# Optimization experiments

Hardware: AMD Instinct MI355X
Metric: run time of the kernel (lower is better)

## Reference

```python
import jax, jax.numpy as jnp
import numpy as np

B, T, E = 2, 2048, 1024
H, D = 16, 64
FF = 4096
EPS = 1e-5


def _layer_norm(x, g, b):
    m = jnp.mean(x, axis=-1, keepdims=True)
    v = jnp.mean(jnp.square(x - m), axis=-1, keepdims=True)
    return (x - m) * jax.lax.rsqrt(v + EPS) * g + b


def setup_inputs() -> dict:
    key = jax.random.key(0)
    ks = jax.random.split(key, 8)
    s = lambda fan_in: 1.0 / np.sqrt(fan_in)
    return {
        "src": jax.random.normal(ks[0], (B, T, E), jnp.float32),
        "Wq": jax.random.normal(ks[1], (E, E), jnp.float32) * s(E),
        "Wk": jax.random.normal(ks[2], (E, E), jnp.float32) * s(E),
        "Wv": jax.random.normal(ks[3], (E, E), jnp.float32) * s(E),
        "Wo": jax.random.normal(ks[4], (E, E), jnp.float32) * s(E),
        "W1": jax.random.normal(ks[5], (2 * FF, E), jnp.float32) * s(E),
        "b1": jnp.zeros((2 * FF,), jnp.float32),
        "W2": jax.random.normal(ks[6], (E, FF), jnp.float32) * s(FF),
        "b2": jnp.zeros((E,), jnp.float32),
        "ln1_w": jnp.ones((E,), jnp.float32),
        "ln1_b": jnp.zeros((E,), jnp.float32),
        "ln2_w": jnp.ones((E,), jnp.float32),
        "ln2_b": jnp.zeros((E,), jnp.float32),
    }


def reference(src, Wq, Wk, Wv, Wo, W1, b1, W2, b2, ln1_w, ln1_b, ln2_w, ln2_b):
    # --- pre-norm self-attention block ---
    h = _layer_norm(src, ln1_w, ln1_b)                       # [B,T,E]
    q = (h @ Wq.T).reshape(B, T, H, D)                       # [B,T,H,D]
    k = (h @ Wk.T).reshape(B, T, H, D)
    v = (h @ Wv.T).reshape(B, T, H, D)
    scores = jnp.einsum("bqhd,bkhd->bhqk", q, k) / np.sqrt(D)
    probs = jax.nn.softmax(scores, axis=-1)                  # [B,H,T,T]
    attn = jnp.einsum("bhqk,bkhd->bqhd", probs, v).reshape(B, T, E)
    x = src + attn @ Wo.T                                    # residual (dropout=0)
    # --- pre-norm GEGLU FFN block ---
    h2 = _layer_norm(x, ln2_w, ln2_b)
    u = h2 @ W1.T + b1                                       # [B,T,2*FF]
    a, gates = jnp.split(u, 2, axis=-1)
    f = a * jax.nn.gelu(gates, approximate=False)            # GEGLU (exact erf gelu)
    return x + (f @ W2.T + b2)
```

## Files before the change

kernel.cpp:

```cpp
#include <hip/hip_runtime.h>
#include <stdint.h>
#include <math.h>

#define DEVI __device__ __forceinline__

typedef __attribute__((ext_vector_type(8))) short sv8;
typedef __attribute__((ext_vector_type(4))) short sv4;
typedef __attribute__((ext_vector_type(4))) float fv4;

typedef __attribute__((address_space(1))) void av1_t;
typedef __attribute__((address_space(3))) void av3_t;

constexpr int Bb = 2, Tt = 2048, Ee = 1024, Hh = 16, Dd = 64, FFd = 4096;
constexpr int NN = Bb * Tt;
constexpr float EPSv = 1e-5f;

#define WAIT_VM(n) asm volatile("s_waitcnt vmcnt(" #n ")" ::: "memory")

DEVI float b2f(unsigned short s) {
  union { unsigned u; float f; } v; v.u = ((unsigned)s) << 16; return v.f;
}
DEVI unsigned short f2b(float f) {
  union { float f; unsigned u; } v; v.f = f;
  return (unsigned short)((v.u + 0x7FFFu + ((v.u >> 16) & 1u)) >> 16);
}
DEVI unsigned short f2b_rtz(float f) {
  union { float f; unsigned u; } v; v.f = f;
  return (unsigned short)(v.u >> 16);
}

DEVI void load_lds16(const void* g, void* s) {
  __builtin_amdgcn_global_load_lds((av1_t*)(unsigned long long)g,
                                   (av3_t*)(unsigned)(unsigned long long)s,
                                   16, 0, 0);
}

__global__ __launch_bounds__(256) void cvt_kernel(const float* __restrict__ in,
                                                  unsigned short* __restrict__ out, int n,
                                                  float scale) {
  int i = (blockIdx.x * 256 + threadIdx.x) * 4;
  if (i >= n) return;
  float4 v = *(const float4*)(in + i);
  sv4 o;
  o[0] = (short)f2b(v.x * scale); o[1] = (short)f2b(v.y * scale);
  o[2] = (short)f2b(v.z * scale); o[3] = (short)f2b(v.w * scale);
  *(sv4*)(out + i) = o;
}

__global__ __launch_bounds__(256) void cvt_w1_kernel(const float* __restrict__ in,
                                                     unsigned short* __restrict__ out) {
  int i = (blockIdx.x * 256 + threadIdx.x) * 4;
  const int r = i >> 10, c = i & 1023;
  const int rp = (r < FFd) ? ((r >> 4) * 32 + (r & 15))
                           : (((r - FFd) >> 4) * 32 + 16 + (r & 15));
  float4 v = *(const float4*)(in + i);
  sv4 o;
  o[0] = (short)f2b(v.x); o[1] = (short)f2b(v.y);
  o[2] = (short)f2b(v.z); o[3] = (short)f2b(v.w);
  *(sv4*)(out + (size_t)rp * Ee + c) = o;
}

__global__ __launch_bounds__(256) void vt_kernel(const unsigned short* __restrict__ qkv,
                                                 unsigned short* __restrict__ vT) {
  const int bh = blockIdx.y;
  const int b = bh >> 4, h = bh & 15;
  const int tt = blockIdx.x * 64;
  const int tid = threadIdx.x;
  __shared__ unsigned short tile[64][65];
  const int tr = tid >> 2, tc4 = (tid & 3) * 16;
  const unsigned short* src = qkv + (size_t)(b * Tt + tt + tr) * (3 * Ee) + 2 * Ee + h * 64 + tc4;
  const sv8 a0 = *(const sv8*)src;
  const sv8 a1 = *(const sv8*)(src + 8);
#pragma unroll
  for (int j = 0; j < 8; ++j) { tile[tr][tc4 + j] = a0[j]; tile[tr][tc4 + 8 + j] = a1[j]; }
  __syncthreads();
  unsigned short* dst = vT + ((size_t)bh * 64 + tr) * Tt + tt + tc4;
  sv8 o0, o1;
#pragma unroll
  for (int j = 0; j < 8; ++j) { o0[j] = (short)tile[tc4 + j][tr]; o1[j] = (short)tile[tc4 + 8 + j][tr]; }
  *(sv8*)dst = o0;
  *(sv8*)(dst + 8) = o1;
}

__global__ __launch_bounds__(256) void ln_kernel(const float* __restrict__ x,
                                                 const float* __restrict__ g,
                                                 const float* __restrict__ b,
                                                 unsigned short* __restrict__ out) {
  const int row = blockIdx.x, tid = threadIdx.x;
  const float4 v = *(const float4*)(x + (size_t)row * Ee + tid * 4);
  float s = v.x + v.y + v.z + v.w;
  float ss = v.x * v.x + v.y * v.y + v.z * v.z + v.w * v.w;
#pragma unroll
  for (int off = 32; off; off >>= 1) { s += __shfl_down(s, off); ss += __shfl_down(ss, off); }
  __shared__ float red[16];
  const int w = tid >> 6, l = tid & 63;
  if (l == 0) { red[w] = s; red[8 + w] = ss; }
  __syncthreads();
  s = red[0] + red[1] + red[2] + red[3];
  ss = red[8] + red[9] + red[10] + red[11];
  const float mean = s * (1.f / Ee);
  const float rstd = rsqrtf(ss * (1.f / Ee) - mean * mean + EPSv);
  const float4 gv = *(const float4*)(g + tid * 4);
  const float4 bv = *(const float4*)(b + tid * 4);
  sv4 o;
  o[0] = (short)f2b((v.x - mean) * rstd * gv.x + bv.x);
  o[1] = (short)f2b((v.y - mean) * rstd * gv.y + bv.y);
  o[2] = (short)f2b((v.z - mean) * rstd * gv.z + bv.z);
  o[3] = (short)f2b((v.w - mean) * rstd * gv.w + bv.w);
  *(sv4*)(out + (size_t)row * Ee + tid * 4) = o;
}

template <int OUTF32, int HASBIAS, int BN, int GEGLU>
__global__ __launch_bounds__(256) void gemm_bt(const unsigned short* __restrict__ A,
                                               const unsigned short* __restrict__ Bw,
                                               void* __restrict__ Cout,
                                               const float* __restrict__ bias,
                                               const float* __restrict__ res,
                                               int M, int K) {
  constexpr int NI = BN / 32;
  __shared__ unsigned short lA[3][128 * 32];
  __shared__ unsigned short lB[3][BN * 32];
  const int tid = threadIdx.x;
  const int l = tid & 63, w = tid >> 6;
  const int wr = w >> 1, wc = w & 1;
  const int rowbase = blockIdx.y * 128, colbase = blockIdx.x * BN;

  const fv4 zero4 = {0.f, 0.f, 0.f, 0.f};
  fv4 acc[4][NI];
#pragma unroll
  for (int i = 0; i < 4; ++i)
#pragma unroll
    for (int j = 0; j < NI; ++j) acc[i][j] = zero4;

  const int c0 = tid, c1 = tid + 256;
  const int sw0 = ((c0 & 3) ^ ((c0 >> 3) & 3)) * 8;
  const int sw1 = ((c1 & 3) ^ ((c1 >> 3) & 3)) * 8;
  const unsigned short* Ag0 = A + (size_t)(rowbase + (c0 >> 2)) * K + sw0;
  const unsigned short* Ag1 = A + (size_t)(rowbase + (c1 >> 2)) * K + sw1;
  const unsigned short* Bg0 = Bw + (size_t)(colbase + (c0 >> 2)) * K + sw0;
  const unsigned short* Bg1 = Bw + (size_t)(colbase + ((BN == 128 ? c1 : c0) >> 2)) * K +
                              (BN == 128 ? sw1 : sw0);

  const int nk = K >> 5;

  auto stage = [&](int buf) {
    load_lds16(Ag0, lA[buf] + c0 * 8);
    load_lds16(Ag1, lA[buf] + c1 * 8);
    load_lds16(Bg0, lB[buf] + c0 * 8);
    if (BN == 128) load_lds16(Bg1, lB[buf] + c1 * 8);
    Ag0 += 32; Ag1 += 32; Bg0 += 32; Bg1 += 32;
  };

  stage(0);
  stage(1);
  if constexpr (BN == 128) WAIT_VM(4); else WAIT_VM(3);
  __builtin_amdgcn_s_barrier();

  int cur = 0;
  for (int t = 0; t < nk; ++t) {
    const int pf = (cur + 2 >= 3) ? cur - 1 : cur + 2;
    if (t + 2 < nk) stage(pf);
    sv8 af[4], bfr[NI];
#pragma unroll
    for (int i = 0; i < 4; ++i) {
      const int ra = wr * 64 + i * 16 + (l & 15);
      af[i] = *(const sv8*)(lA[cur] + ra * 32 + (((l >> 4) ^ ((ra >> 1) & 3)) * 8));
    }
#pragma unroll
    for (int i = 0; i < NI; ++i) {
      const int rb = wc * (BN / 2) + i * 16 + (l & 15);
      bfr[i] = *(const sv8*)(lB[cur] + rb * 32 + (((l >> 4) ^ ((rb >> 1) & 3)) * 8));
    }
    __builtin_amdgcn_s_setprio(1);
#pragma unroll
    for (int mi = 0; mi < 4; ++mi)
#pragma unroll
      for (int ni = 0; ni < NI; ++ni)
        acc[mi][ni] = __builtin_amdgcn_mfma_f32_16x16x32_bf16(af[mi], bfr[ni], acc[mi][ni], 0, 0, 0);
    __builtin_amdgcn_s_setprio(0);
    if (t + 2 < nk) {
      if constexpr (BN == 128) WAIT_VM(4); else WAIT_VM(3);
      __builtin_amdgcn_s_barrier();
    } else if (t + 1 < nk) {
      WAIT_VM(0);
      __builtin_amdgcn_s_barrier();
    }
    cur = (cur + 1 >= 3) ? 0 : cur + 1;
  }

  const int r0 = rowbase + wr * 64 + ((l >> 4) * 4);
  const int ccol = colbase + wc * (BN / 2) + (l & 15);
#pragma unroll
  for (int mi = 0; mi < 4; ++mi) {
#pragma unroll
    for (int j = 0; j < 4; ++j) {
      const size_t r = (size_t)(r0 + mi * 16 + j);
      if (GEGLU) {
#pragma unroll
        for (int p = 0; p < NI / 2; ++p) {
          const int ca = ccol + p * 32;
          const int ocol = ((ca >> 5) << 4) | (ca & 15);
          const float av = acc[mi][2 * p][j] + bias[ocol];
          const float gv = acc[mi][2 * p + 1][j] + bias[ocol + (M >> 1)];
          const float y = 0.7978845608028654f * (gv + 0.044715f * gv * gv * gv);
          const float e = exp2f(2.8853900817779268f * y);
          const float gel = gv * (1.f - 1.f / (e + 1.f));
          ((unsigned short*)Cout)[r * (size_t)(M >> 1) + ocol] = f2b(av * gel);
        }
      } else {
#pragma unroll
        for (int ni = 0; ni < NI; ++ni) {
          const int c = ccol + ni * 16;
          float vv = acc[mi][ni][j];
          if (HASBIAS) vv += bias[c];
          if (OUTF32) {
            ((float*)Cout)[r * M + c] = res[r * M + c] + vv;
          } else {
            ((unsigned short*)Cout)[r * M + c] = f2b(vv);
          }
        }
      }
    }
  }
}

__global__ __launch_bounds__(256) void attn_kernel(const unsigned short* __restrict__ Q,
                                                   const unsigned short* __restrict__ Kb,
                                                   const unsigned short* __restrict__ vT,
                                                   unsigned short* __restrict__ O,
                                                   int ld) {
  const int bidl = ((blockIdx.x & 7) << 7) + (blockIdx.x >> 3);
  const int bh = bidl >> 5;
  const int b = bh / Hh, h = bh % Hh;
  const int q0 = (bidl & 31) * 64;
  const int tid = threadIdx.x, l = tid & 63, w = tid >> 6;
  const size_t base = (size_t)b * Tt * ld + (size_t)h * Dd;
  const size_t baseO = (size_t)b * Tt * Ee + (size_t)h * Dd;
  const unsigned short* vTb = vT + (size_t)bh * 64 * Tt;

  __shared__ unsigned short Kt[2][64 * 64];
  __shared__ unsigned short Vt[2][64 * 64];
  __shared__ unsigned short Pt[4][16 * 64];

  sv8 qf0, qf1;
  {
    const unsigned short* qp = Q + base + (size_t)(q0 + w * 16 + (l & 15)) * ld + (l >> 4) * 8;
    qf0 = *(const sv8*)qp;
    qf1 = *(const sv8*)(qp + 32);
  }

  const fv4 zero4 = {0.f, 0.f, 0.f, 0.f};
  fv4 acc_o[4];
#pragma unroll
  for (int i = 0; i < 4; ++i) acc_o[i] = zero4;
  float Mx = -INFINITY;
  float Lp[4];
#pragma unroll
  for (int j = 0; j < 4; ++j) Lp[j] = 0.f;

  const int c0 = tid, c1 = tid + 256;
  const int r0c = c0 >> 3, xc0 = c0 & 7;
  const int r1c = c1 >> 3, xc1 = c1 & 7;

  load_lds16(Kb + base + (size_t)(r0c)*ld + (xc0 ^ (r0c & 7)) * 8, Kt[0] + c0 * 8);
  load_lds16(Kb + base + (size_t)(r1c)*ld + (xc1 ^ (r1c & 7)) * 8, Kt[0] + c1 * 8);
  load_lds16(vTb + (size_t)(r0c)*Tt + (xc0 ^ (r0c & 7)) * 8, Vt[0] + c0 * 8);
  load_lds16(vTb + (size_t)(r1c)*Tt + (xc1 ^ (r1c & 7)) * 8, Vt[0] + c1 * 8);
  __syncthreads();

  int cur = 0;
  for (int kt = 0; kt < Tt / 64; ++kt) {
    const int nx = cur ^ 1;
    if (kt + 1 < Tt / 64) {
      load_lds16(Kb + base + (size_t)((kt + 1) * 64 + r0c) * ld + (xc0 ^ (r0c & 7)) * 8, Kt[nx] + c0 * 8);
      load_lds16(Kb + base + (size_t)((kt + 1) * 64 + r1c) * ld + (xc1 ^ (r1c & 7)) * 8, Kt[nx] + c1 * 8);
      load_lds16(vTb + (size_t)(r0c)*Tt + (kt + 1) * 64 + (xc0 ^ (r0c & 7)) * 8, Vt[nx] + c0 * 8);
      load_lds16(vTb + (size_t)(r1c)*Tt + (kt + 1) * 64 + (xc1 ^ (r1c & 7)) * 8, Vt[nx] + c1 * 8);
    }

    fv4 s[4];
    __builtin_amdgcn_s_setprio(1);
#pragma unroll
    for (int ks = 0; ks < 4; ++ks) {
      const int row = ks * 16 + (l & 15);
      const sv8 kf0 = *(const sv8*)(Kt[cur] + row * 64 + (((l >> 4) ^ (row & 7)) * 8));
      const sv8 kf1 = *(const sv8*)(Kt[cur] + row * 64 + (((4 + (l >> 4)) ^ (row & 7)) * 8));
      fv4 t = zero4;
      t = __builtin_amdgcn_mfma_f32_16x16x32_bf16(qf0, kf0, t, 0, 0, 0);
      t = __builtin_amdgcn_mfma_f32_16x16x32_bf16(qf1, kf1, t, 0, 0, 0);
      s[ks] = t;
    }
    __builtin_amdgcn_s_setprio(0);

    float m01 = fmaxf(fmaxf(s[0][0], s[0][1]), fmaxf(s[0][2], s[0][3]));
    float m1 = fmaxf(fmaxf(s[1][0], s[1][1]), fmaxf(s[1][2], s[1][3]));
    float m2 = fmaxf(fmaxf(s[2][0], s[2][1]), fmaxf(s[2][2], s[2][3]));
    float m3 = fmaxf(fmaxf(s[3][0], s[3][1]), fmaxf(s[3][2], s[3][3]));
    float tm = fmaxf(fmaxf(m01, m1), fmaxf(m2, m3));
    if (__any(tm > Mx + 11.5f)) {
      float mt = tm;
#pragma unroll
      for (int off = 1; off < 16; off <<= 1) mt = fmaxf(mt, __shfl_xor(mt, off, 16));
      const float mnew = fmaxf(Mx, mt);
      const float alpha = exp2f(Mx - mnew);
      Mx = mnew;
#pragma unroll
      for (int j = 0; j < 4; ++j) {
        Lp[j] *= alpha;
#pragma unroll
        for (int dsb = 0; dsb < 4; ++dsb) acc_o[dsb][j] *= alpha;
      }
    }
#pragma unroll
    for (int ks = 0; ks < 4; ++ks)
#pragma unroll
      for (int j = 0; j < 4; ++j) {
        const float p = exp2f(s[ks][j] - Mx);
        s[ks][j] = p;
        Lp[j] += p;
      }
#pragma unroll
    for (int ks = 0; ks < 4; ++ks)
#pragma unroll
      for (int j = 0; j < 4; ++j) {
        const int q = (l >> 4) * 4 + j, k = ks * 16 + (l & 15);
        Pt[w][q * 64 + ((((k >> 3) ^ (q & 7)) & 7) * 8) + (k & 7)] = f2b_rtz(s[ks][j]);
      }
    asm volatile("s_waitcnt lgkmcnt(0)" ::: "memory");

    __builtin_amdgcn_s_setprio(1);
#pragma unroll
    for (int kcn = 0; kcn < 2; ++kcn) {
      const int qr = l & 15;
      const sv8 pf = *(const sv8*)(&Pt[w][qr * 64 + (((kcn * 4 + (l >> 4)) ^ (qr & 7)) * 8)]);
#pragma unroll
      for (int dsb = 0; dsb < 4; ++dsb) {
        const int row = dsb * 16 + (l & 15);
        const int chunk = kcn * 4 + (l >> 4);
        const sv8 vf = *(const sv8*)(Vt[cur] + row * 64 + ((chunk ^ (row & 7)) * 8));
        acc_o[dsb] = __builtin_amdgcn_mfma_f32_16x16x32_bf16(pf, vf, acc_o[dsb], 0, 0, 0);
      }
    }
    __builtin_amdgcn_s_setprio(0);

    __syncthreads();
    cur = nx;
  }

#pragma unroll
  for (int j = 0; j < 4; ++j) {
    float t = Lp[j];
#pragma unroll
    for (int off = 1; off < 16; off <<= 1) t += __shfl_xor(t, off, 16);
    const float inv = 1.f / t;
    unsigned short* op = O + baseO + (size_t)(q0 + w * 16 + (l >> 4) * 4 + j) * Ee;
#pragma unroll
    for (int dsb = 0; dsb < 4; ++dsb)
      op[dsb * 16 + (l & 15)] = f2b(acc_o[dsb][j] * inv);
  }
}

extern "C" void kernel_launch(void* const* d_in, const int* in_sizes, int n_in,
                              void* d_out, int out_size, void* d_ws, size_t ws_size,
                              hipStream_t stream) {
  (void)in_sizes; (void)n_in; (void)out_size; (void)ws_size;
  const float* src  = (const float*)d_in[0];
  const float* Wq   = (const float*)d_in[1];
  const float* Wk   = (const float*)d_in[2];
  const float* Wv   = (const float*)d_in[3];
  const float* Wo   = (const float*)d_in[4];
  const float* W1   = (const float*)d_in[5];
  const float* b1   = (const float*)d_in[6];
  const float* W2   = (const float*)d_in[7];
  const float* b2   = (const float*)d_in[8];
  const float* ln1w = (const float*)d_in[9];
  const float* ln1b = (const float*)d_in[10];
  const float* ln2w = (const float*)d_in[11];
  const float* ln2b = (const float*)d_in[12];
  float* out = (float*)d_out;

  char* ws = (char*)d_ws;
  size_t off = 0;
  auto alloc = [&](size_t bytes) { char* p = ws + off; off += bytes; return p; };
  unsigned short* wqkv = (unsigned short*)alloc((size_t)3 * Ee * Ee * 2);
  unsigned short* wo16 = (unsigned short*)alloc((size_t)Ee * Ee * 2);
  unsigned short* w116 = (unsigned short*)alloc((size_t)2 * FFd * Ee * 2);
  unsigned short* w216 = (unsigned short*)alloc((size_t)Ee * FFd * 2);
  unsigned short* h16  = (unsigned short*)alloc((size_t)NN * Ee * 2);
  unsigned short* qkv  = (unsigned short*)alloc((size_t)NN * 3 * Ee * 2);
  unsigned short* a16  = (unsigned short*)alloc((size_t)NN * Ee * 2);
  float* xbuf          = (float*)alloc((size_t)NN * Ee * 4);
  unsigned short* vT   = (unsigned short*)alloc((size_t)NN * Ee * 2);
  unsigned short* f16  = qkv;

  const float s2 = 0.125f * 1.4426950408889634f;

  dim3 blk(256);
  cvt_kernel<<<dim3(Ee * Ee / 1024), blk, 0, stream>>>(Wq, wqkv, Ee * Ee, s2);
  cvt_kernel<<<dim3(Ee * Ee / 1024), blk, 0, stream>>>(Wk, wqkv + Ee * Ee, Ee * Ee, 1.0f);
  cvt_kernel<<<dim3(Ee * Ee / 1024), blk, 0, stream>>>(Wv, wqkv + 2 * Ee * Ee, Ee * Ee, 1.0f);
  cvt_kernel<<<dim3(Ee * Ee / 1024), blk, 0, stream>>>(Wo, wo16, Ee * Ee, 1.0f);
  cvt_w1_kernel<<<dim3(2 * FFd * Ee / 1024), blk, 0, stream>>>(W1, w116);
  cvt_kernel<<<dim3(Ee * FFd / 1024), blk, 0, stream>>>(W2, w216, Ee * FFd, 1.0f);

  ln_kernel<<<dim3(NN), blk, 0, stream>>>(src, ln1w, ln1b, h16);

  gemm_bt<0, 0, 128, 0><<<dim3(3 * Ee / 128, NN / 128), blk, 0, stream>>>(h16, wqkv, qkv, nullptr, nullptr, 3 * Ee, Ee);

  vt_kernel<<<dim3(Tt / 64, Bb * Hh), blk, 0, stream>>>(qkv, vT);

  attn_kernel<<<dim3(1024), blk, 0, stream>>>(qkv, qkv + Ee, vT, a16, 3 * Ee);

  gemm_bt<1, 0, 64, 0><<<dim3(Ee / 64, NN / 128), blk, 0, stream>>>(a16, wo16, xbuf, nullptr, src, Ee, Ee);

  ln_kernel<<<dim3(NN), blk, 0, stream>>>(xbuf, ln2w, ln2b, h16);

  gemm_bt<0, 0, 128, 1><<<dim3(2 * FFd / 128, NN / 128), blk, 0, stream>>>(h16, w116, f16, b1, nullptr, 2 * FFd, Ee);

  gemm_bt<1, 1, 64, 0><<<dim3(Ee / 64, NN / 128), blk, 0, stream>>>(f16, w216, out, b2, xbuf, Ee, FFd);
}
```

Baseline: 315.3 us.

## Add 256x256-tile 512-thread GEMM with fused GEGLU for FFN up-projection

```diff
diff --git a/kernel.cpp b/kernel.cpp
--- a/kernel.cpp
+++ b/kernel.cpp
@@ -218,6 +218,142 @@
           } else {
             ((unsigned short*)Cout)[r * M + c] = f2b(vv);
           }
+        }
+      }
+    }
+  }
+}
+
+template <int GEGLU>
+__global__ __launch_bounds__(512, 2) void gemm256(const unsigned short* __restrict__ A,
+                                                  const unsigned short* __restrict__ Bw,
+                                                  void* __restrict__ Cout,
+                                                  const float* __restrict__ bias,
+                                                  int M, int K) {
+  __shared__ unsigned short Ah[2][2][256 * 32];
+  __shared__ unsigned short Bh[2][2][256 * 32];
+  const int tid = threadIdx.x;
+  const int l = tid & 63, w = tid >> 6;
+  const int wrow = w >> 2, wcol = w & 3;
+  const int nbase = blockIdx.y * 256, mbase = blockIdx.x * 256;
+
+  const fv4 zero4 = {0.f, 0.f, 0.f, 0.f};
+  fv4 acc[8][4];
+#pragma unroll
+  for (int i = 0; i < 8; ++i)
+#pragma unroll
+    for (int j = 0; j < 4; ++j) acc[i][j] = zero4;
+
+  const int s0 = tid, s1 = tid + 512;
+  const int r0 = s0 >> 2, x0 = (((s0 & 3) ^ ((r0 >> 1) & 3))) * 8;
+  const int r1 = s1 >> 2, x1 = (((s1 & 3) ^ ((r1 >> 1) & 3))) * 8;
+  const unsigned short* As0 = A + (size_t)(nbase + r0) * K + x0;
+  const unsigned short* As1 = A + (size_t)(nbase + r1) * K + x1;
+  const unsigned short* Bs0 = Bw + (size_t)(mbase + r0) * K + x0;
+  const unsigned short* Bs1 = Bw + (size_t)(mbase + r1) * K + x1;
+
+  const int nk = K >> 6;
+
+  auto stA = [&](int db, int kh, int kof) {
+    load_lds16(As0 + kof + kh * 32, &Ah[db][kh][s0 * 8]);
+    load_lds16(As1 + kof + kh * 32, &Ah[db][kh][s1 * 8]);
+  };
+  auto stB = [&](int db, int kh, int kof) {
+    load_lds16(Bs0 + kof + kh * 32, &Bh[db][kh][s0 * 8]);
+    load_lds16(Bs1 + kof + kh * 32, &Bh[db][kh][s1 * 8]);
+  };
+
+  const int cl = (((l >> 4) ^ ((l >> 1) & 3))) * 8;
+  const int arl = (wrow * 128 + (l & 15)) * 32 + cl;
+  const int brl = (wcol * 64 + (l & 15)) * 32 + cl;
+
+  stA(0, 0, 0); stB(0, 0, 0); stA(0, 1, 0); stB(0, 1, 0);
+
+  for (int t = 0; t < nk; ++t) {
+    const int st = t & 1, sf = st ^ 1;
+    const int kof = (t + 1) * 64;
+    const bool pre = (t + 1 < nk);
+    sv8 af[8], b0, b1;
+
+    WAIT_VM(4);
+    __builtin_amdgcn_s_barrier();
+    __builtin_amdgcn_sched_barrier(0);
+    if (pre) stA(sf, 0, kof);
+#pragma unroll
+    for (int mi = 0; mi < 8; ++mi) af[mi] = *(const sv8*)(&Ah[st][0][arl + mi * 512]);
+    b0 = *(const sv8*)(&Bh[st][0][brl]);
+    b1 = *(const sv8*)(&Bh[st][0][brl + 512]);
+    __builtin_amdgcn_s_setprio(1);
+#pragma unroll
+    for (int mi = 0; mi < 8; ++mi) {
+      acc[mi][0] = __builtin_amdgcn_mfma_f32_16x16x32_bf16(af[mi], b0, acc[mi][0], 0, 0, 0);
+      acc[mi][1] = __builtin_amdgcn_mfma_f32_16x16x32_bf16(af[mi], b1, acc[mi][1], 0, 0, 0);
+    }
+    __builtin_amdgcn_s_setprio(0);
+
+    if (pre) stB(sf, 0, kof);
+    b0 = *(const sv8*)(&Bh[st][0][brl + 2 * 512]);
+    b1 = *(const sv8*)(&Bh[st][0][brl + 3 * 512]);
+    __builtin_amdgcn_s_setprio(1);
+#pragma unroll
+    for (int mi = 0; mi < 8; ++mi) {
+      acc[mi][2] = __builtin_amdgcn_mfma_f32_16x16x32_bf16(af[mi], b0, acc[mi][2], 0, 0, 0);
+      acc[mi][3] = __builtin_amdgcn_mfma_f32_16x16x32_bf16(af[mi], b1, acc[mi][3], 0, 0, 0);
+    }
+    __builtin_amdgcn_s_setprio(0);
+
+    if (pre) { WAIT_VM(4); } else { WAIT_VM(0); }
+    __builtin_amdgcn_s_barrier();
+    __builtin_amdgcn_sched_barrier(0);
+    if (pre) stA(sf, 1, kof);
+#pragma unroll
+    for (int mi = 0; mi < 8; ++mi) af[mi] = *(const sv8*)(&Ah[st][1][arl + mi * 512]);
+    b0 = *(const sv8*)(&Bh[st][1][brl]);
+    b1 = *(const sv8*)(&Bh[st][1][brl + 512]);
+    __builtin_amdgcn_s_setprio(1);
+#pragma unroll
+    for (int mi = 0; mi < 8; ++mi) {
+      acc[mi][0] = __builtin_amdgcn_mfma_f32_16x16x32_bf16(af[mi], b0, acc[mi][0], 0, 0, 0);
+      acc[mi][1] = __builtin_amdgcn_mfma_f32_16x16x32_bf16(af[mi], b1, acc[mi][1], 0, 0, 0);
+    }
+    __builtin_amdgcn_s_setprio(0);
+
+    if (pre) stB(sf, 1, kof);
+    b0 = *(const sv8*)(&Bh[st][1][brl + 2 * 512]);
+    b1 = *(const sv8*)(&Bh[st][1][brl + 3 * 512]);
+    __builtin_amdgcn_s_setprio(1);
+#pragma unroll
+    for (int mi = 0; mi < 8; ++mi) {
+      acc[mi][2] = __builtin_amdgcn_mfma_f32_16x16x32_bf16(af[mi], b0, acc[mi][2], 0, 0, 0);
+      acc[mi][3] = __builtin_amdgcn_mfma_f32_16x16x32_bf16(af[mi], b1, acc[mi][3], 0, 0, 0);
+    }
+    __builtin_amdgcn_s_setprio(0);
+  }
+
+  const int rbase = nbase + wrow * 128 + ((l >> 4) * 4);
+  const int cbase = mbase + wcol * 64 + (l & 15);
+#pragma unroll
+  for (int mi = 0; mi < 8; ++mi) {
+#pragma unroll
+    for (int j = 0; j < 4; ++j) {
+      const size_t r = (size_t)(rbase + mi * 16 + j);
+      if (GEGLU) {
+#pragma unroll
+        for (int p = 0; p < 2; ++p) {
+          const int ca = cbase + p * 32;
+          const int ocol = ((ca >> 5) << 4) | (ca & 15);
+          const float av = acc[mi][2 * p][j] + bias[ocol];
+          const float gv = acc[mi][2 * p + 1][j] + bias[ocol + (M >> 1)];
+          const float y = 0.7978845608028654f * (gv + 0.044715f * gv * gv * gv);
+          const float e = exp2f(2.8853900817779268f * y);
+          const float gel = gv * (1.f - 1.f / (e + 1.f));
+          ((unsigned short*)Cout)[r * (size_t)(M >> 1) + ocol] = f2b(av * gel);
+        }
+      } else {
+#pragma unroll
+        for (int ni = 0; ni < 4; ++ni) {
+          const int c = cbase + ni * 16;
+          ((unsigned short*)Cout)[r * (size_t)M + c] = f2b(acc[mi][ni][j]);
         }
       }
     }
@@ -415,7 +551,7 @@
 
   ln_kernel<<<dim3(NN), blk, 0, stream>>>(xbuf, ln2w, ln2b, h16);
 
-  gemm_bt<0, 0, 128, 1><<<dim3(2 * FFd / 128, NN / 128), blk, 0, stream>>>(h16, w116, f16, b1, nullptr, 2 * FFd, Ee);
+  gemm256<1><<<dim3(2 * FFd / 256, NN / 256), dim3(512), 0, stream>>>(h16, w116, f16, b1, 2 * FFd, Ee);
 
   gemm_bt<1, 1, 64, 0><<<dim3(Ee / 64, NN / 128), blk, 0, stream>>>(f16, w216, out, b2, xbuf, Ee, FFd);
 }
```

Measured after the change: 302.0 us. 1.04x faster.
